# Performance work log

Hardware: AMD Instinct MI355X
Metric: run time of the kernel (lower is better)

## Reference

```python
import jax, jax.numpy as jnp
import numpy as np

EPSILON = 1e-15
LOG2 = 0.6931471805599453
N_VARS = 4096
BATCH = 512
OUT_SIZES = [16384, 8192, 4096, 2048]
FANINS = [4, 2, 4, 2]


def log1mexp(x):
    # accurate log(1 - exp(x)) for x < 0
    return jnp.where(x > -LOG2,
                     jnp.log(-jnp.expm1(x)),
                     jnp.log1p(-jnp.exp(x)))


def encode_input(pos):
    # rows: [-inf, 0, pos0, neg0, pos1, neg1, ...]
    neg = log1mexp(pos)
    inter = jnp.stack([pos, neg], axis=1).reshape(2 * pos.shape[0], pos.shape[1])
    head = jnp.stack([jnp.full(pos.shape[1:], -jnp.inf, pos.dtype),
                      jnp.zeros(pos.shape[1:], pos.dtype)])
    return jnp.concatenate([head, inter], axis=0)


def product_layer(x, ptrs, seg, n_out):
    return jax.ops.segment_sum(x[ptrs], seg, num_segments=n_out)


def sum_layer(x, ptrs, seg, n_out):
    g = x[ptrs]
    a = jax.lax.stop_gradient(jax.ops.segment_max(g, seg, num_segments=n_out))
    s = jax.ops.segment_sum(jnp.exp(g - a[seg]), seg, num_segments=n_out)
    return jnp.log(s + EPSILON) + a


def setup_inputs() -> dict:
    rng = np.random.default_rng(0)
    # log-probabilities in (-inf, 0): pos = log(u), u in (0,1)
    u = rng.uniform(1e-4, 1.0 - 1e-4, size=(N_VARS, BATCH)).astype(np.float32)
    x = jnp.asarray(np.log(u))

    inputs = {"x": x}
    prev_size = 2 * N_VARS + 2
    for i, (n_out, fanin) in enumerate(zip(OUT_SIZES, FANINS)):
        n_edges = n_out * fanin
        lo = 1 if i == 0 else 0  # avoid the -inf constant row at layer 0
        ptrs = rng.integers(lo, prev_size, size=n_edges).astype(np.int64)
        seg = np.repeat(np.arange(n_out, dtype=np.int64), fanin)
        inputs[f"ptrs{i}"] = jnp.asarray(ptrs)
        inputs[f"seg{i}"] = jnp.asarray(seg)
        prev_size = n_out
    return inputs


def reference(x, ptrs0, seg0, ptrs1, seg1, ptrs2, seg2, ptrs3, seg3):
    h = encode_input(x)
    ptrs = [ptrs0, ptrs1, ptrs2, ptrs3]
    segs = [seg0, seg1, seg2, seg3]
    for i, n_out in enumerate(OUT_SIZES):
        if i % 2 == 0:
            h = product_layer(h, ptrs[i], segs[i], n_out)
        else:
            h = sum_layer(h, ptrs[i], segs[i], n_out)
    return h
```

## Files before the change

### kernel.cpp

```cpp
#include <hip/hip_runtime.h>
#include <math.h>

#define BATCH    512
#define N_VARS   4096
#define H_ROWS   (2 * N_VARS + 2)
#define N_OUT1   8192
#define N_OUT3   2048
#define TPB      1024
#define SMEM_BYTES (H_ROWS * sizeof(float2))

__device__ __forceinline__ float log1mexp_fast(float x) {
    return __logf(1.0f - __expf(x));
}

__device__ __forceinline__ float2 lse2_fast2(float2 a, float2 b) {
    float2 r;
    r.x = fmaxf(a.x, b.x) + __logf(1.0f + __expf(-fabsf(a.x - b.x)));
    r.y = fmaxf(a.y, b.y) + __logf(1.0f + __expf(-fabsf(a.y - b.y)));
    return r;
}

__global__ void build_tabs_kernel(const int* __restrict__ p0,
                                  const int* __restrict__ p1,
                                  const int* __restrict__ p2,
                                  const int* __restrict__ p3,
                                  int4* __restrict__ tabB,
                                  int4* __restrict__ tabC) {
    int o = blockIdx.x * blockDim.x + threadIdx.x;
    if (o < N_OUT1) {
        int2 pp = ((const int2*)p1)[o];
        tabB[2 * o]     = ((const int4*)p0)[pp.x];
        tabB[2 * o + 1] = ((const int4*)p0)[pp.y];
    } else {
        int oc = o - N_OUT1;
        int2 pp = ((const int2*)p3)[oc];
        tabC[2 * oc]     = ((const int4*)p2)[pp.x];
        tabC[2 * oc + 1] = ((const int4*)p2)[pp.y];
    }
}

__global__ void __launch_bounds__(TPB, 4)
fused_spn_kernel(const float* __restrict__ x,
                 const int4* __restrict__ tabB,
                 const int4* __restrict__ tabC,
                 float* __restrict__ out) {
    extern __shared__ float2 buf[];
    const int bp = blockIdx.x;
    const int t = threadIdx.x;
    const float2* x2 = (const float2*)x;

    if (t == 0) {
        buf[0] = make_float2(-INFINITY, -INFINITY);
        buf[1] = make_float2(0.f, 0.f);
    }
#pragma unroll
    for (int k = 0; k < N_VARS / TPB; ++k) {
        int i = t + k * TPB;
        float2 p = x2[(size_t)i * (BATCH / 2) + bp];
        buf[2 * i + 2] = p;
        buf[2 * i + 3] = make_float2(log1mexp_fast(p.x), log1mexp_fast(p.y));
    }
    __syncthreads();

    float2 r1[N_OUT1 / TPB];
#pragma unroll
    for (int c = 0; c < N_OUT1 / TPB; c += 4) {
        int4 qa[4], qb[4];
#pragma unroll
        for (int k = 0; k < 4; ++k) {
            int o = t + (c + k) * TPB;
            qa[k] = tabB[2 * o];
            qb[k] = tabB[2 * o + 1];
        }
#pragma unroll
        for (int k = 0; k < 4; ++k) {
            float2 va0 = buf[qa[k].x], va1 = buf[qa[k].y];
            float2 va2 = buf[qa[k].z], va3 = buf[qa[k].w];
            float2 vb0 = buf[qb[k].x], vb1 = buf[qb[k].y];
            float2 vb2 = buf[qb[k].z], vb3 = buf[qb[k].w];
            float2 ga = make_float2(va0.x + va1.x + va2.x + va3.x,
                                    va0.y + va1.y + va2.y + va3.y);
            float2 gb = make_float2(vb0.x + vb1.x + vb2.x + vb3.x,
                                    vb0.y + vb1.y + vb2.y + vb3.y);
            r1[c + k] = lse2_fast2(ga, gb);
        }
    }
    __syncthreads();
#pragma unroll
    for (int k = 0; k < N_OUT1 / TPB; ++k)
        buf[t + k * TPB] = r1[k];
    __syncthreads();

    {
        int4 qa[2], qb[2];
#pragma unroll
        for (int k = 0; k < 2; ++k) {
            int o = t + k * TPB;
            qa[k] = tabC[2 * o];
            qb[k] = tabC[2 * o + 1];
        }
#pragma unroll
        for (int k = 0; k < 2; ++k) {
            int o = t + k * TPB;
            float2 va0 = buf[qa[k].x], va1 = buf[qa[k].y];
            float2 va2 = buf[qa[k].z], va3 = buf[qa[k].w];
            float2 vb0 = buf[qb[k].x], vb1 = buf[qb[k].y];
            float2 vb2 = buf[qb[k].z], vb3 = buf[qb[k].w];
            float2 ga = make_float2(va0.x + va1.x + va2.x + va3.x,
                                    va0.y + va1.y + va2.y + va3.y);
            float2 gb = make_float2(vb0.x + vb1.x + vb2.x + vb3.x,
                                    vb0.y + vb1.y + vb2.y + vb3.y);
            ((float2*)(out + (size_t)o * BATCH))[bp] = lse2_fast2(ga, gb);
        }
    }
}

extern "C" void kernel_launch(void* const* d_in, const int* in_sizes, int n_in,
                              void* d_out, int out_size, void* d_ws, size_t ws_size,
                              hipStream_t stream) {
    const float* x     = (const float*)d_in[0];
    const int*   ptrs0 = (const int*)d_in[1];
    const int*   ptrs1 = (const int*)d_in[3];
    const int*   ptrs2 = (const int*)d_in[5];
    const int*   ptrs3 = (const int*)d_in[7];
    float* out = (float*)d_out;

    int4* tabB = (int4*)d_ws;
    int4* tabC = tabB + 2 * N_OUT1;

    hipFuncSetAttribute((const void*)fused_spn_kernel,
                        hipFuncAttributeMaxDynamicSharedMemorySize, SMEM_BYTES);

    build_tabs_kernel<<<(N_OUT1 + N_OUT3) / 256, 256, 0, stream>>>(
        ptrs0, ptrs1, ptrs2, ptrs3, tabB, tabC);

    fused_spn_kernel<<<BATCH / 2, TPB, SMEM_BYTES, stream>>>(x, tabB, tabC, out);
}
```

Baseline: 94.73 us.

## Transpose input in prep kernel for coalesced per-block loads

Adds a tiled shared-memory transpose of x (variables × batch into batch × variables) inside the table-building kernel, merging both jobs into one launch. The fused kernel then reads each block's two batch columns with contiguous float4 loads instead of 8-byte strided loads. This removes uncoalesced global reads in the main kernel. In exchange the full 8 MB input is read and written once more, the workspace grows, and the shared-memory writes of the encoded rows become strided by eight float2 per thread.

```diff
diff --git a/kernel.cpp b/kernel.cpp
--- a/kernel.cpp
+++ b/kernel.cpp
@@ -20,45 +20,70 @@
     return r;
 }
 
-__global__ void build_tabs_kernel(const int* __restrict__ p0,
-                                  const int* __restrict__ p1,
-                                  const int* __restrict__ p2,
-                                  const int* __restrict__ p3,
-                                  int4* __restrict__ tabB,
-                                  int4* __restrict__ tabC) {
-    int o = blockIdx.x * blockDim.x + threadIdx.x;
-    if (o < N_OUT1) {
-        int2 pp = ((const int2*)p1)[o];
-        tabB[2 * o]     = ((const int4*)p0)[pp.x];
-        tabB[2 * o + 1] = ((const int4*)p0)[pp.y];
+#define TDIM    32
+#define NTRANS  ((BATCH / TDIM) * (N_VARS / TDIM))
+#define NTAB    ((N_OUT1 + N_OUT3) / 256)
+__global__ void prep_kernel(const float* __restrict__ x,
+                            float* __restrict__ xT,
+                            const int* __restrict__ p0,
+                            const int* __restrict__ p1,
+                            const int* __restrict__ p2,
+                            const int* __restrict__ p3,
+                            int4* __restrict__ tabB,
+                            int4* __restrict__ tabC) {
+    __shared__ float tile[TDIM][TDIM + 1];
+    int blk = blockIdx.x;
+    int tx = threadIdx.x, ty = threadIdx.y;
+    if (blk < NTRANS) {
+        int cb = (blk % (BATCH / TDIM)) * TDIM;
+        int rb = (blk / (BATCH / TDIM)) * TDIM;
+#pragma unroll
+        for (int j = 0; j < TDIM; j += 8)
+            tile[ty + j][tx] = x[(size_t)(rb + ty + j) * BATCH + cb + tx];
+        __syncthreads();
+#pragma unroll
+        for (int j = 0; j < TDIM; j += 8)
+            xT[(size_t)(cb + ty + j) * N_VARS + rb + tx] = tile[tx][ty + j];
     } else {
-        int oc = o - N_OUT1;
-        int2 pp = ((const int2*)p3)[oc];
-        tabC[2 * oc]     = ((const int4*)p2)[pp.x];
-        tabC[2 * oc + 1] = ((const int4*)p2)[pp.y];
+        int o = (blk - NTRANS) * 256 + ty * TDIM + tx;
+        if (o < N_OUT1) {
+            int2 pp = ((const int2*)p1)[o];
+            tabB[2 * o]     = ((const int4*)p0)[pp.x];
+            tabB[2 * o + 1] = ((const int4*)p0)[pp.y];
+        } else {
+            int oc = o - N_OUT1;
+            int2 pp = ((const int2*)p3)[oc];
+            tabC[2 * oc]     = ((const int4*)p2)[pp.x];
+            tabC[2 * oc + 1] = ((const int4*)p2)[pp.y];
+        }
     }
 }
 
 __global__ void __launch_bounds__(TPB, 4)
-fused_spn_kernel(const float* __restrict__ x,
+fused_spn_kernel(const float* __restrict__ xT,
                  const int4* __restrict__ tabB,
                  const int4* __restrict__ tabC,
                  float* __restrict__ out) {
     extern __shared__ float2 buf[];
     const int bp = blockIdx.x;
     const int t = threadIdx.x;
-    const float2* x2 = (const float2*)x;
 
     if (t == 0) {
         buf[0] = make_float2(-INFINITY, -INFINITY);
         buf[1] = make_float2(0.f, 0.f);
     }
-#pragma unroll
-    for (int k = 0; k < N_VARS / TPB; ++k) {
-        int i = t + k * TPB;
-        float2 p = x2[(size_t)i * (BATCH / 2) + bp];
-        buf[2 * i + 2] = p;
-        buf[2 * i + 3] = make_float2(log1mexp_fast(p.x), log1mexp_fast(p.y));
+    {
+        float4 pa = ((const float4*)(xT + (size_t)(2 * bp)     * N_VARS))[t];
+        float4 pb = ((const float4*)(xT + (size_t)(2 * bp + 1) * N_VARS))[t];
+        int base = 8 * t + 2;
+        buf[base + 0] = make_float2(pa.x, pb.x);
+        buf[base + 1] = make_float2(log1mexp_fast(pa.x), log1mexp_fast(pb.x));
+        buf[base + 2] = make_float2(pa.y, pb.y);
+        buf[base + 3] = make_float2(log1mexp_fast(pa.y), log1mexp_fast(pb.y));
+        buf[base + 4] = make_float2(pa.z, pb.z);
+        buf[base + 5] = make_float2(log1mexp_fast(pa.z), log1mexp_fast(pb.z));
+        buf[base + 6] = make_float2(pa.w, pb.w);
+        buf[base + 7] = make_float2(log1mexp_fast(pa.w), log1mexp_fast(pb.w));
     }
     __syncthreads();
 
@@ -125,14 +150,15 @@
     const int*   ptrs3 = (const int*)d_in[7];
     float* out = (float*)d_out;
 
-    int4* tabB = (int4*)d_ws;
-    int4* tabC = tabB + 2 * N_OUT1;
+    float* xT  = (float*)d_ws;
+    int4*  tabB = (int4*)(xT + (size_t)N_VARS * BATCH);
+    int4*  tabC = tabB + 2 * N_OUT1;
 
     hipFuncSetAttribute((const void*)fused_spn_kernel,
                         hipFuncAttributeMaxDynamicSharedMemorySize, SMEM_BYTES);
 
-    build_tabs_kernel<<<(N_OUT1 + N_OUT3) / 256, 256, 0, stream>>>(
-        ptrs0, ptrs1, ptrs2, ptrs3, tabB, tabC);
+    prep_kernel<<<NTRANS + NTAB, dim3(32, 8), 0, stream>>>(
+        x, xT, ptrs0, ptrs1, ptrs2, ptrs3, tabB, tabC);
 
-    fused_spn_kernel<<<BATCH / 2, TPB, SMEM_BYTES, stream>>>(x, tabB, tabC, out);
+    fused_spn_kernel<<<BATCH / 2, TPB, SMEM_BYTES, stream>>>(xT, tabB, tabC, out);
 }
```

New measurement: 89.09 us. 1.06x faster.
